# Performance work log

Measured on AMD Instinct MI355X. Metric: run time of the kernel, lower is better.

The kernel has to match this reference:

```python
import jax, jax.numpy as jnp
import numpy as np

CHANNELS = 1024
PIVOT = 16384


def setup_inputs() -> dict:
    key = jax.random.key(0)
    k1, k2, k3 = jax.random.split(key, 3)
    x_Jx = jax.random.normal(k1, (3 * PIVOT, CHANNELS), dtype=jnp.float32)
    # Linear(channels, channels) params, torch-like init scale
    s = 1.0 / np.sqrt(CHANNELS)
    W = jax.random.uniform(k2, (CHANNELS, CHANNELS), dtype=jnp.float32, minval=-s, maxval=s)
    b = jax.random.uniform(k3, (CHANNELS,), dtype=jnp.float32, minval=-s, maxval=s)
    return {"x_Jx": x_Jx, "W": W, "b": b}


def reference(x_Jx, W, b):
    pivot = x_Jx.shape[0] // 3
    channels = W.shape[0]
    x = x_Jx[:pivot]                                   # [P, C]
    hAx = jnp.tanh(x @ W.T + b)                        # [P, C]
    hpAx = 1.0 - hAx ** 2                              # tanh'
    Jx = x_Jx[pivot:].reshape(pivot, channels, 2)      # [P, C, 2]
    # sum_j W[i,j] * Jx[p,j,k]  (the explicit broadcast-sum in torch is this GEMM)
    WJx = jnp.einsum('ij,pjk->pik', W, Jx)             # [P, C, 2]
    hpAJx = (hpAx[:, :, None] * WJx).reshape(-1, channels)  # [2P, C]
    return jnp.concatenate([hAx, hpAJx], axis=0)       # [3P, C]
```

## Files before the change

### kernel.cpp

```cpp
#include <hip/hip_runtime.h>
#include <hip/hip_bf16.h>
#include <cstdint>

typedef __attribute__((ext_vector_type(8))) short short8;
typedef __attribute__((ext_vector_type(4))) float floatx4;

__device__ __forceinline__ float tanh_fast(float x) {
    float e = __expf(2.0f * x);
    return 1.0f - 2.0f * __builtin_amdgcn_rcpf(e + 1.0f);
}

__device__ __forceinline__ unsigned int bf16_bits(float f) {
    __hip_bfloat16 h = __float2bfloat16(f);
    return (unsigned int)*reinterpret_cast<unsigned short*>(&h);
}
__device__ __forceinline__ unsigned int pack2(float lo, float hi) {
    return bf16_bits(lo) | (bf16_bits(hi) << 16);
}

#define LDS_STRIDE 72

__global__ __launch_bounds__(256) void k1_gemm_tanh(
    const float* __restrict__ X,
    const float* __restrict__ W,
    const float* __restrict__ Bv,
    float* __restrict__ out,
    int K)
{
    __shared__ __align__(16) short As[128 * LDS_STRIDE];
    __shared__ __align__(16) short Bs[128 * LDS_STRIDE];

    const int tid  = threadIdx.x;
    const int lane = tid & 63;
    const int wave = tid >> 6;
    const int wm = wave & 1, wn = wave >> 1;

    const int row0 = blockIdx.y * 128;
    const int col0 = blockIdx.x * 128;

    const int l15  = lane & 15;
    const int quad = lane >> 4;
    const int a_base = (wm * 64 + l15) * LDS_STRIDE;
    const int b_base = (wn * 64 + l15) * LDS_STRIDE;

    floatx4 acc[4][4];
#pragma unroll
    for (int a = 0; a < 4; ++a)
#pragma unroll
        for (int b = 0; b < 4; ++b) acc[a][b] = (floatx4){0.f, 0.f, 0.f, 0.f};

    for (int k0 = 0; k0 < K; k0 += 64) {
        __syncthreads();
#pragma unroll
        for (int i = 0; i < 8; ++i) {
            const int g = i * 256 + tid;
            const int r = g >> 4, c = g & 15;
            const float4 va = *(const float4*)(X + (size_t)(row0 + r) * K + k0 + c * 4);
            const float4 vb = *(const float4*)(W + (size_t)(col0 + r) * K + k0 + c * 4);
            uint2 ea, eb;
            ea.x = pack2(va.x, va.y); ea.y = pack2(va.z, va.w);
            eb.x = pack2(vb.x, vb.y); eb.y = pack2(vb.z, vb.w);
            *(uint2*)&As[r * LDS_STRIDE + c * 4] = ea;
            *(uint2*)&Bs[r * LDS_STRIDE + c * 4] = eb;
        }
        __syncthreads();
#pragma unroll
        for (int ki = 0; ki < 2; ++ki) {
            const int kx = ki * 32 + quad * 8;
            short8 af[4], bf[4];
#pragma unroll
            for (int s = 0; s < 4; ++s)
                af[s] = *(const short8*)&As[a_base + s * 16 * LDS_STRIDE + kx];
#pragma unroll
            for (int s = 0; s < 4; ++s)
                bf[s] = *(const short8*)&Bs[b_base + s * 16 * LDS_STRIDE + kx];
#pragma unroll
            for (int a = 0; a < 4; ++a)
#pragma unroll
                for (int b = 0; b < 4; ++b)
                    acc[a][b] = __builtin_amdgcn_mfma_f32_16x16x32_bf16(
                        af[a], bf[b], acc[a][b], 0, 0, 0);
        }
    }

    float bv[4];
#pragma unroll
    for (int b = 0; b < 4; ++b)
        bv[b] = Bv[col0 + wn * 64 + b * 16 + l15];

#pragma unroll
    for (int a = 0; a < 4; ++a) {
        const int rbase = row0 + wm * 64 + a * 16 + quad * 4;
#pragma unroll
        for (int b = 0; b < 4; ++b) {
            const int n = col0 + wn * 64 + b * 16 + l15;
#pragma unroll
            for (int r = 0; r < 4; ++r)
                out[(size_t)(rbase + r) * 1024 + n] = tanh_fast(acc[a][b][r] + bv[b]);
        }
    }
}

__global__ __launch_bounds__(256) void k2_gemm_jac(
    const float* __restrict__ G,
    const float* __restrict__ W,
    const float* __restrict__ Hout,
    float* __restrict__ out2,
    int K)
{
    __shared__ __align__(16) short As[128 * LDS_STRIDE];
    __shared__ __align__(16) short Bs[128 * LDS_STRIDE];

    const int tid  = threadIdx.x;
    const int lane = tid & 63;
    const int wave = tid >> 6;
    const int wm = wave & 1, wn = wave >> 1;

    const int r0   = blockIdx.y * 128;
    const int p0   = r0 >> 1;
    const int col0 = blockIdx.x * 128;

    const int l15  = lane & 15;
    const int quad = lane >> 4;
    const int a_base = (wm * 64 + l15) * LDS_STRIDE;
    const int b_base = (wn * 64 + l15) * LDS_STRIDE;

    floatx4 acc[4][4];
#pragma unroll
    for (int a = 0; a < 4; ++a)
#pragma unroll
        for (int b = 0; b < 4; ++b) acc[a][b] = (floatx4){0.f, 0.f, 0.f, 0.f};

    for (int k0 = 0; k0 < K; k0 += 64) {
        __syncthreads();
#pragma unroll
        for (int i = 0; i < 8; ++i) {
            const int g = i * 256 + tid;
            const int r = g >> 4, c = g & 15;
            const float4 vb = *(const float4*)(W + (size_t)(col0 + r) * K + k0 + c * 4);
            uint2 eb;
            eb.x = pack2(vb.x, vb.y); eb.y = pack2(vb.z, vb.w);
            *(uint2*)&Bs[r * LDS_STRIDE + c * 4] = eb;
        }
#pragma unroll
        for (int i = 0; i < 4; ++i) {
            const int g = i * 256 + tid;
            const int q = g >> 4, d = g & 15;
            const float* src = G + (size_t)(p0 + q) * 2048 + 2 * k0 + d * 8;
            const float4 u0 = *(const float4*)src;
            const float4 u1 = *(const float4*)(src + 4);
            uint2 E, O;
            E.x = pack2(u0.x, u0.z); E.y = pack2(u1.x, u1.z);
            O.x = pack2(u0.y, u0.w); O.y = pack2(u1.y, u1.w);
            *(uint2*)&As[(2 * q)     * LDS_STRIDE + d * 4] = E;
            *(uint2*)&As[(2 * q + 1) * LDS_STRIDE + d * 4] = O;
        }
        __syncthreads();
#pragma unroll
        for (int ki = 0; ki < 2; ++ki) {
            const int kx = ki * 32 + quad * 8;
            short8 af[4], bf[4];
#pragma unroll
            for (int s = 0; s < 4; ++s)
                af[s] = *(const short8*)&As[a_base + s * 16 * LDS_STRIDE + kx];
#pragma unroll
            for (int s = 0; s < 4; ++s)
                bf[s] = *(const short8*)&Bs[b_base + s * 16 * LDS_STRIDE + kx];
#pragma unroll
            for (int a = 0; a < 4; ++a)
#pragma unroll
                for (int b = 0; b < 4; ++b)
                    acc[a][b] = __builtin_amdgcn_mfma_f32_16x16x32_bf16(
                        af[a], bf[b], acc[a][b], 0, 0, 0);
        }
    }

#pragma unroll
    for (int a = 0; a < 4; ++a) {
        const int rb = r0 + wm * 64 + a * 16 + quad * 4;
#pragma unroll
        for (int b = 0; b < 4; ++b) {
            const int i = col0 + wn * 64 + b * 16 + l15;
            const int shift = (i >= 512) ? 1 : 0;
            const int ccol = 2 * i - shift * 1024;
#pragma unroll
            for (int pr = 0; pr < 2; ++pr) {
                const int re = rb + pr * 2;
                const int p  = re >> 1;
                const float h  = Hout[(size_t)p * 1024 + i];
                const float hp = 1.0f - h * h;
                float2 st;
                st.x = hp * acc[a][b][pr * 2];
                st.y = hp * acc[a][b][pr * 2 + 1];
                *(float2*)&out2[(size_t)(re + shift) * 1024 + ccol] = st;
            }
        }
    }
}

extern "C" void kernel_launch(void* const* d_in, const int* in_sizes, int n_in,
                              void* d_out, int out_size, void* d_ws, size_t ws_size,
                              hipStream_t stream) {
    const float* xJx = (const float*)d_in[0];
    const float* W   = (const float*)d_in[1];
    const float* bv  = (const float*)d_in[2];
    float* out = (float*)d_out;

    const int C     = 1024;
    const int rows3 = in_sizes[0] / C;
    const int pivot = rows3 / 3;

    dim3 blk(256);
    dim3 g1(C / 128, pivot / 128);
    k1_gemm_tanh<<<g1, blk, 0, stream>>>(xJx, W, bv, out, C);

    dim3 g2(C / 128, (2 * pivot) / 128);
    k2_gemm_jac<<<g2, blk, 0, stream>>>(xJx + (size_t)pivot * C, W, out,
                                        out + (size_t)pivot * C, C);
}
```

Measured before the change: 539.3 us.

## Prefetch next K-tile into registers, swizzle tile order, add nontemporal stores

Both GEMM kernels now load the next 64-wide K slice of global data into registers while the current slice is converted and consumed through LDS, so global load latency can overlap with MFMA work. Workgroup-to-tile mapping is swizzled so concurrently running blocks share W column tiles and input rows in cache. Launch bounds request 3 blocks per CU, and output writes plus the Hout reads use nontemporal hints. The register prefetch buffers raise register pressure, which may cause spills or lower occupancy under the occupancy hint.

Result: slower. 718.2 us (+33.2%).

```diff
diff --git a/kernel.cpp b/kernel.cpp
--- a/kernel.cpp
+++ b/kernel.cpp
@@ -4,6 +4,7 @@
 
 typedef __attribute__((ext_vector_type(8))) short short8;
 typedef __attribute__((ext_vector_type(4))) float floatx4;
+typedef __attribute__((ext_vector_type(2))) float floatx2;
 
 __device__ __forceinline__ float tanh_fast(float x) {
     float e = __expf(2.0f * x);
@@ -20,7 +21,15 @@
 
 #define LDS_STRIDE 72
 
-__global__ __launch_bounds__(256) void k1_gemm_tanh(
+__device__ __forceinline__ void swizzle_tile(int& row0, int& col0) {
+    const int nwg  = gridDim.x * gridDim.y;
+    const int flat = blockIdx.y * gridDim.x + blockIdx.x;
+    const int swz  = (flat & 7) * (nwg >> 3) + (flat >> 3);
+    col0 = (swz & 7) * 128;
+    row0 = (swz >> 3) * 128;
+}
+
+__global__ __launch_bounds__(256, 3) void k1_gemm_tanh(
     const float* __restrict__ X,
     const float* __restrict__ W,
     const float* __restrict__ Bv,
@@ -35,33 +44,50 @@
     const int wave = tid >> 6;
     const int wm = wave & 1, wn = wave >> 1;
 
-    const int row0 = blockIdx.y * 128;
-    const int col0 = blockIdx.x * 128;
+    int row0, col0;
+    swizzle_tile(row0, col0);
 
     const int l15  = lane & 15;
     const int quad = lane >> 4;
     const int a_base = (wm * 64 + l15) * LDS_STRIDE;
     const int b_base = (wn * 64 + l15) * LDS_STRIDE;
 
+    const int sr = tid >> 4;
+    const int sc = tid & 15;
+    const float* Xp = X + (size_t)(row0 + sr) * K + sc * 4;
+    const float* Wp = W + (size_t)(col0 + sr) * K + sc * 4;
+
     floatx4 acc[4][4];
 #pragma unroll
     for (int a = 0; a < 4; ++a)
 #pragma unroll
         for (int b = 0; b < 4; ++b) acc[a][b] = (floatx4){0.f, 0.f, 0.f, 0.f};
 
+    float4 pa[8], pb[8];
+
+#pragma unroll
+    for (int i = 0; i < 8; ++i) {
+        pa[i] = *(const float4*)(Xp + (size_t)i * 16 * K);
+        pb[i] = *(const float4*)(Wp + (size_t)i * 16 * K);
+    }
+
     for (int k0 = 0; k0 < K; k0 += 64) {
         __syncthreads();
 #pragma unroll
         for (int i = 0; i < 8; ++i) {
-            const int g = i * 256 + tid;
-            const int r = g >> 4, c = g & 15;
-            const float4 va = *(const float4*)(X + (size_t)(row0 + r) * K + k0 + c * 4);
-            const float4 vb = *(const float4*)(W + (size_t)(col0 + r) * K + k0 + c * 4);
+            const int r = i * 16 + sr;
             uint2 ea, eb;
-            ea.x = pack2(va.x, va.y); ea.y = pack2(va.z, va.w);
-            eb.x = pack2(vb.x, vb.y); eb.y = pack2(vb.z, vb.w);
-            *(uint2*)&As[r * LDS_STRIDE + c * 4] = ea;
-            *(uint2*)&Bs[r * LDS_STRIDE + c * 4] = eb;
+            ea.x = pack2(pa[i].x, pa[i].y); ea.y = pack2(pa[i].z, pa[i].w);
+            eb.x = pack2(pb[i].x, pb[i].y); eb.y = pack2(pb[i].z, pb[i].w);
+            *(uint2*)&As[r * LDS_STRIDE + sc * 4] = ea;
+            *(uint2*)&Bs[r * LDS_STRIDE + sc * 4] = eb;
+        }
+        if (k0 + 64 < K) {
+#pragma unroll
+            for (int i = 0; i < 8; ++i) {
+                pa[i] = *(const float4*)(Xp + (size_t)i * 16 * K + k0 + 64);
+                pb[i] = *(const float4*)(Wp + (size_t)i * 16 * K + k0 + 64);
+            }
         }
         __syncthreads();
 #pragma unroll
@@ -96,12 +122,14 @@
             const int n = col0 + wn * 64 + b * 16 + l15;
 #pragma unroll
             for (int r = 0; r < 4; ++r)
-                out[(size_t)(rbase + r) * 1024 + n] = tanh_fast(acc[a][b][r] + bv[b]);
-        }
-    }
-}
-
-__global__ __launch_bounds__(256) void k2_gemm_jac(
+                __builtin_nontemporal_store(
+                    tanh_fast(acc[a][b][r] + bv[b]),
+                    &out[(size_t)(rbase + r) * 1024 + n]);
+        }
+    }
+}
+
+__global__ __launch_bounds__(256, 3) void k2_gemm_jac(
     const float* __restrict__ G,
     const float* __restrict__ W,
     const float* __restrict__ Hout,
@@ -116,44 +144,67 @@
     const int wave = tid >> 6;
     const int wm = wave & 1, wn = wave >> 1;
 
-    const int r0   = blockIdx.y * 128;
-    const int p0   = r0 >> 1;
-    const int col0 = blockIdx.x * 128;
+    int r0, col0;
+    swizzle_tile(r0, col0);
+    const int p0 = r0 >> 1;
 
     const int l15  = lane & 15;
     const int quad = lane >> 4;
     const int a_base = (wm * 64 + l15) * LDS_STRIDE;
     const int b_base = (wn * 64 + l15) * LDS_STRIDE;
 
+    const int sr = tid >> 4;
+    const int sc = tid & 15;
+    const float* Wp = W + (size_t)(col0 + sr) * K + sc * 4;
+    const float* Gp = G + (size_t)(p0 + sr) * 2048 + sc * 8;
+
     floatx4 acc[4][4];
 #pragma unroll
     for (int a = 0; a < 4; ++a)
 #pragma unroll
         for (int b = 0; b < 4; ++b) acc[a][b] = (floatx4){0.f, 0.f, 0.f, 0.f};
 
+    float4 pb[8];
+    float4 qa[4][2];
+
+#pragma unroll
+    for (int i = 0; i < 8; ++i)
+        pb[i] = *(const float4*)(Wp + (size_t)i * 16 * K);
+#pragma unroll
+    for (int i = 0; i < 4; ++i) {
+        const float* src = Gp + (size_t)i * 16 * 2048;
+        qa[i][0] = *(const float4*)src;
+        qa[i][1] = *(const float4*)(src + 4);
+    }
+
     for (int k0 = 0; k0 < K; k0 += 64) {
         __syncthreads();
 #pragma unroll
         for (int i = 0; i < 8; ++i) {
-            const int g = i * 256 + tid;
-            const int r = g >> 4, c = g & 15;
-            const float4 vb = *(const float4*)(W + (size_t)(col0 + r) * K + k0 + c * 4);
+            const int r = i * 16 + sr;
             uint2 eb;
-            eb.x = pack2(vb.x, vb.y); eb.y = pack2(vb.z, vb.w);
-            *(uint2*)&Bs[r * LDS_STRIDE + c * 4] = eb;
+            eb.x = pack2(pb[i].x, pb[i].y); eb.y = pack2(pb[i].z, pb[i].w);
+            *(uint2*)&Bs[r * LDS_STRIDE + sc * 4] = eb;
         }
 #pragma unroll
         for (int i = 0; i < 4; ++i) {
-            const int g = i * 256 + tid;
-            const int q = g >> 4, d = g & 15;
-            const float* src = G + (size_t)(p0 + q) * 2048 + 2 * k0 + d * 8;
-            const float4 u0 = *(const float4*)src;
-            const float4 u1 = *(const float4*)(src + 4);
+            const int q = i * 16 + sr;
             uint2 E, O;
-            E.x = pack2(u0.x, u0.z); E.y = pack2(u1.x, u1.z);
-            O.x = pack2(u0.y, u0.w); O.y = pack2(u1.y, u1.w);
-            *(uint2*)&As[(2 * q)     * LDS_STRIDE + d * 4] = E;
-            *(uint2*)&As[(2 * q + 1) * LDS_STRIDE + d * 4] = O;
+            E.x = pack2(qa[i][0].x, qa[i][0].z); E.y = pack2(qa[i][1].x, qa[i][1].z);
+            O.x = pack2(qa[i][0].y, qa[i][0].w); O.y = pack2(qa[i][1].y, qa[i][1].w);
+            *(uint2*)&As[(2 * q)     * LDS_STRIDE + sc * 4] = E;
+            *(uint2*)&As[(2 * q + 1) * LDS_STRIDE + sc * 4] = O;
+        }
+        if (k0 + 64 < K) {
+#pragma unroll
+            for (int i = 0; i < 8; ++i)
+                pb[i] = *(const float4*)(Wp + (size_t)i * 16 * K + k0 + 64);
+#pragma unroll
+            for (int i = 0; i < 4; ++i) {
+                const float* src = Gp + (size_t)i * 16 * 2048 + 2 * (k0 + 64);
+                qa[i][0] = *(const float4*)src;
+                qa[i][1] = *(const float4*)(src + 4);
+            }
         }
         __syncthreads();
 #pragma unroll
@@ -187,12 +238,14 @@
             for (int pr = 0; pr < 2; ++pr) {
                 const int re = rb + pr * 2;
                 const int p  = re >> 1;
-                const float h  = Hout[(size_t)p * 1024 + i];
+                const float h  = __builtin_nontemporal_load(
+                                     &Hout[(size_t)p * 1024 + i]);
                 const float hp = 1.0f - h * h;
-                float2 st;
+                floatx2 st;
                 st.x = hp * acc[a][b][pr * 2];
                 st.y = hp * acc[a][b][pr * 2 + 1];
-                *(float2*)&out2[(size_t)(re + shift) * 1024 + ccol] = st;
+                __builtin_nontemporal_store(
+                    st, (floatx2*)&out2[(size_t)(re + shift) * 1024 + ccol]);
             }
         }
     }
```
